# Kernel optimization log

Measured on AMD Instinct MI355X. Metric: run time of the kernel, lower is better.

## Reference

```python
import jax, jax.numpy as jnp
import numpy as np

DEPTH, HEADS, DIM_HEAD, DIM, MLP, PATCH_DIM, NP_, NC = 8, 8, 64, 512, 2048, 512, 1024, 2
INNER = HEADS * DIM_HEAD
SCALE = DIM_HEAD ** -0.5
EPS = 1e-5

def layernorm(x, s, b):
    m = x.mean(-1, keepdims=True)
    v = ((x - m) ** 2).mean(-1, keepdims=True)
    return (x - m) * jax.lax.rsqrt(v + EPS) * s + b

def setup_inputs() -> dict:
    key = jax.random.key(0)
    ks = jax.random.split(key, 24)
    g = lambda k, sh, sc=0.02: jax.random.normal(k, sh, dtype=jnp.float32) * sc
    return {
        "img": jax.random.normal(ks[0], (4, NP_, PATCH_DIM), dtype=jnp.float32),
        "embed_w": g(ks[1], (PATCH_DIM, DIM)), "embed_b": jnp.zeros((DIM,), jnp.float32),
        "pos_emb": g(ks[2], (1, NP_ + 1, DIM), 1.0), "cls_token": g(ks[3], (1, 1, DIM), 1.0),
        "ln1_s": jnp.ones((DEPTH, DIM), jnp.float32), "ln1_b": jnp.zeros((DEPTH, DIM), jnp.float32),
        "qkv_w": g(ks[4], (DEPTH, DIM, 3 * INNER)),
        "out_w": g(ks[5], (DEPTH, INNER, DIM)), "out_b": jnp.zeros((DEPTH, DIM), jnp.float32),
        "ln2_s": jnp.ones((DEPTH, DIM), jnp.float32), "ln2_b": jnp.zeros((DEPTH, DIM), jnp.float32),
        "ff_w1": g(ks[6], (DEPTH, DIM, MLP)), "ff_b1": jnp.zeros((DEPTH, MLP), jnp.float32),
        "ff_w2": g(ks[7], (DEPTH, MLP, DIM)), "ff_b2": jnp.zeros((DEPTH, DIM), jnp.float32),
        "head_ln_s": jnp.ones((DIM,), jnp.float32), "head_ln_b": jnp.zeros((DIM,), jnp.float32),
        "head_w": g(ks[8], (DIM, NC)), "head_b": jnp.zeros((NC,), jnp.float32),
    }

def reference(img, embed_w, embed_b, pos_emb, cls_token, ln1_s, ln1_b, qkv_w, out_w, out_b,
              ln2_s, ln2_b, ff_w1, ff_b1, ff_w2, ff_b2, head_ln_s, head_ln_b, head_w, head_b):
    B, N, _ = img.shape
    x = img @ embed_w + embed_b                       # [B, N, DIM]
    cls = jnp.broadcast_to(cls_token, (B, 1, DIM))
    x = jnp.concatenate([cls, x], axis=1) + pos_emb[:, :N + 1]
    for l in range(DEPTH):
        h = layernorm(x, ln1_s[l], ln1_b[l])
        qkv = h @ qkv_w[l]                            # [B, N+1, 3*INNER]
        q, k, v = jnp.split(qkv, 3, axis=-1)
        rh = lambda t: t.reshape(B, N + 1, HEADS, DIM_HEAD).transpose(0, 2, 1, 3)
        q, k, v = rh(q), rh(k), rh(v)                 # [B, H, N+1, Dh]
        dots = jnp.einsum('bhnd,bhmd->bhnm', q, k) * SCALE
        attn = jax.nn.softmax(dots, axis=-1)
        o = jnp.einsum('bhnm,bhmd->bhnd', attn, v)
        o = o.transpose(0, 2, 1, 3).reshape(B, N + 1, INNER)
        x = o @ out_w[l] + out_b[l] + x
        h = layernorm(x, ln2_s[l], ln2_b[l])
        h = jax.nn.gelu(h @ ff_w1[l] + ff_b1[l], approximate=False)
        x = h @ ff_w2[l] + ff_b2[l] + x
    x = x[:, 0]                                       # cls pooling
    x = layernorm(x, head_ln_s, head_ln_b)
    return (jax.nn.sigmoid(x @ head_w + head_b),)
```

## Files before the change

### kernel.cpp

```cpp
#include <hip/hip_runtime.h>
#include <math.h>
#include <stdint.h>

#define NHEADS   8
#define DHEAD    64
#define DIMM     512
#define MLPD     2048
#define NPATCH   1024
#define NTOK     1025
#define BATCH    4
#define ROWS     (BATCH*NTOK)
#define TOKPAD   1088
#define NCHUNK   17
#define CSPLIT   9
#define QSC      0.180336881f
#define LN_EPS   1e-5f

typedef __attribute__((ext_vector_type(8))) short short8;
typedef __attribute__((ext_vector_type(4))) float f32x4;

__device__ __forceinline__ unsigned short f2bf(float f) {
  union { float f; unsigned u; } c; c.f = f;
  unsigned u = c.u;
  return (unsigned short)((u + 0x7fffu + ((u >> 16) & 1u)) >> 16);
}
__device__ __forceinline__ unsigned short f2bf_fast(float f) {
  union { float f; unsigned u; } c; c.f = f;
  return (unsigned short)((c.u + 0x8000u) >> 16);
}
__device__ __forceinline__ float bf2f(unsigned short b) {
  union { unsigned u; float f; } c; c.u = (unsigned)b << 16;
  return c.f;
}

__device__ __forceinline__ float wsum(float v) {
#pragma unroll
  for (int o = 32; o > 0; o >>= 1) v += __shfl_xor(v, o, 64);
  return v;
}

__device__ __forceinline__ void gl_lds16(const void* g, const void* l) {
  __builtin_amdgcn_global_load_lds(
      (const __attribute__((address_space(1))) unsigned int*)(uintptr_t)g,
      (__attribute__((address_space(3))) unsigned int*)(unsigned int)(uintptr_t)l,
      16, 0, 0);
}

template <int TM, int TN, int WR, int WC>
__global__ __launch_bounds__(256) void mgemm_k(
    const unsigned short* __restrict__ A, const unsigned short* __restrict__ Bt,
    const float* __restrict__ bias, const float* __restrict__ res,
    void* __restrict__ Cout, int M, int N, int K, int flags,
    unsigned short* __restrict__ vTout)
{
  constexpr int AF = TM / WR / 16;
  constexpr int BF = TN / WC / 16;
  constexpr int AG = TM / 32;
  constexpr int BG = TN / 32;
  __shared__ unsigned short sA[2][TM * 64];
  __shared__ unsigned short sB[2][TN * 64];
  const int tid = threadIdx.x;
  const int w = tid >> 6, lane = tid & 63;
  const int quad = lane >> 4, l15 = lane & 15;
  const int m0 = blockIdx.y * TM, n0 = blockIdx.x * TN;
  const int wrow = (w / WC) * (TM / WR);
  const int wcol = (w % WC) * (TN / WC);
  const int lrow = lane >> 3;
  const int lkg = (lane & 7) ^ lrow;

  size_t abase[AG], bbase[BG];
#pragma unroll
  for (int g = 0; g < AG; g++) {
    int grp = w * AG + g;
    int ar = m0 + grp * 8 + lrow; ar = ar < M ? ar : M - 1;
    abase[g] = (size_t)ar * K + lkg * 8;
  }
#pragma unroll
  for (int g = 0; g < BG; g++) {
    int grp = w * BG + g;
    int br = n0 + grp * 8 + lrow;
    bbase[g] = (size_t)br * K + lkg * 8;
  }

  auto stage = [&](int k0, int buf) {
#pragma unroll
    for (int g = 0; g < AG; g++)
      gl_lds16(A + abase[g] + k0, &sA[buf][(w * AG + g) * 512]);
#pragma unroll
    for (int g = 0; g < BG; g++)
      gl_lds16(Bt + bbase[g] + k0, &sB[buf][(w * BG + g) * 512]);
  };

  f32x4 acc[AF][BF];
#pragma unroll
  for (int i = 0; i < AF; i++)
#pragma unroll
    for (int j = 0; j < BF; j++) { f32x4 z = {0.f, 0.f, 0.f, 0.f}; acc[i][j] = z; }

  stage(0, 0);
  const int nsteps = K >> 6;
  for (int step = 0; step < nsteps; step++) {
    const int buf = step & 1;
    __syncthreads();
    if (step + 1 < nsteps) stage((step + 1) << 6, buf ^ 1);
#pragma unroll
    for (int kk = 0; kk < 2; kk++) {
      short8 af[AF], bfr[BF];
#pragma unroll
      for (int i = 0; i < AF; i++) {
        int r = wrow + i * 16 + l15;
        af[i] = *(const short8*)&sA[buf][r * 64 + (((kk * 4 + quad) ^ (lane & 7)) << 3)];
      }
#pragma unroll
      for (int j = 0; j < BF; j++) {
        int r = wcol + j * 16 + l15;
        bfr[j] = *(const short8*)&sB[buf][r * 64 + (((kk * 4 + quad) ^ (lane & 7)) << 3)];
      }
#pragma unroll
      for (int i = 0; i < AF; i++)
#pragma unroll
        for (int j = 0; j < BF; j++)
          acc[i][j] = __builtin_amdgcn_mfma_f32_16x16x32_bf16(af[i], bfr[j], acc[i][j], 0, 0, 0);
    }
  }

  const bool do_gelu = flags & 1;
  const bool out_bf  = flags & 2;
#pragma unroll
  for (int i = 0; i < AF; i++) {
#pragma unroll
    for (int j = 0; j < BF; j++) {
      const int col = n0 + wcol + j * 16 + l15;
      const bool vcol = (vTout != nullptr) && (col >= 1024);
      alignas(8) unsigned short vb[4];
#pragma unroll
      for (int rg = 0; rg < 4; rg++) {
        int row = m0 + wrow + i * 16 + quad * 4 + rg;
        if (row >= M) continue;
        float v = acc[i][j][rg];
        if (bias) v += bias[col];
        if (do_gelu) v = 0.5f * v * (1.0f + erff(v * 0.70710678118654752f));
        if (res) v += res[(size_t)row * N + col];
        if (out_bf) {
          unsigned short bv = f2bf(v);
          vb[rg] = bv;
          if (!vcol) ((unsigned short*)Cout)[(size_t)row * N + col] = bv;
        } else {
          ((float*)Cout)[(size_t)row * N + col] = v;
        }
      }
      if (vcol) {
        const int hcol = col - 1024, h = hcol >> 6, d = hcol & 63;
#pragma unroll
        for (int rg = 0; rg < 4; rg++) {
          int row = m0 + wrow + i * 16 + quad * 4 + rg;
          if (row >= M) continue;
          int bb = row / NTOK, tok = row - bb * NTOK;
          vTout[((size_t)(bb * 8 + h) * 64 + d) * TOKPAD + tok] = vb[rg];
        }
      }
    }
  }
}

__global__ __launch_bounds__(256) void attn_k(
    const unsigned short* __restrict__ qkv, const unsigned short* __restrict__ vT,
    unsigned short* __restrict__ po, float* __restrict__ ml)
{
  __shared__ unsigned short ps[64 * 64];
  __shared__ unsigned short ks[2][64 * 64];
  __shared__ unsigned short vs[2][64 * 64];
  const int bh = blockIdx.x, b = bh >> 3, h = bh & 7;
  const int q0 = blockIdx.y * 64;
  const int split = blockIdx.z;
  const int tid = threadIdx.x, w = tid >> 6, lane = tid & 63;
  const int quad = lane >> 4, l15 = lane & 15;
  const int lrow = lane >> 3, lkg = (lane & 7) ^ lrow;
  const unsigned short* qbase = qkv + (size_t)(b * NTOK) * 1536 + h * 64;
  const unsigned short* kbase = qbase + 512;
  const unsigned short* vtb   = vT + (size_t)bh * 64 * TOKPAD;

  auto stage_kv = [&](int c0, int buf) {
#pragma unroll
    for (int g = 0; g < 2; g++) {
      int grp = w * 2 + g;
      int tok = c0 + grp * 8 + lrow; tok = tok < NTOK ? tok : NTOK - 1;
      gl_lds16(kbase + (size_t)tok * 1536 + lkg * 8, &ks[buf][grp * 512]);
      int d = grp * 8 + lrow;
      gl_lds16(vtb + (size_t)d * TOKPAD + c0 + lkg * 8, &vs[buf][grp * 512]);
    }
  };

  const int cbeg = split ? CSPLIT : 0;
  const int cend = split ? NCHUNK : CSPLIT;
  stage_kv(cbeg * 64, 0);

  int qr = q0 + w * 16 + l15; qr = qr < NTOK ? qr : NTOK - 1;
  const unsigned short* qrow = qbase + (size_t)qr * 1536;
  short8 aq[2];
  aq[0] = *(const short8*)(qrow + quad * 8);
  aq[1] = *(const short8*)(qrow + 32 + quad * 8);
#pragma unroll
  for (int k = 0; k < 2; k++)
#pragma unroll
    for (int i = 0; i < 8; i++)
      aq[k][i] = (short)f2bf(bf2f((unsigned short)aq[k][i]) * QSC);

  short8 ones;
#pragma unroll
  for (int i = 0; i < 8; i++) ones[i] = (short)0x3F80;

  f32x4 Oa[4];
#pragma unroll
  for (int n = 0; n < 4; n++) { f32x4 z = {0.f, 0.f, 0.f, 0.f}; Oa[n] = z; }
  float lst[4] = {0.f, 0.f, 0.f, 0.f};

  for (int c = cbeg; c < cend; c++) {
    const int c0 = c * 64;
    const int buf = (c - cbeg) & 1;
    __syncthreads();
    if (c + 1 < cend) stage_kv(c0 + 64, buf ^ 1);

    f32x4 sa[4];
#pragma unroll
    for (int n = 0; n < 4; n++) {
      f32x4 s = {0.f, 0.f, 0.f, 0.f};
#pragma unroll
      for (int kk = 0; kk < 2; kk++) {
        short8 bk = *(const short8*)&ks[buf][(n * 16 + l15) * 64 + (((kk * 4 + quad) ^ (lane & 7)) << 3)];
        s = __builtin_amdgcn_mfma_f32_16x16x32_bf16(aq[kk], bk, s, 0, 0, 0);
      }
      sa[n] = s;
    }

    if (c0 + 64 > NTOK) {
#pragma unroll
      for (int n = 0; n < 4; n++) {
        bool oob = (c0 + n * 16 + l15) >= NTOK;
#pragma unroll
        for (int rg = 0; rg < 4; rg++)
          if (oob) sa[n][rg] = -1e30f;
      }
    }

#pragma unroll
    for (int n = 0; n < 4; n++)
#pragma unroll
      for (int rg = 0; rg < 4; rg++) {
        int row = w * 16 + quad * 4 + rg;
        int key = n * 16 + l15;
        ps[row * 64 + ((((key >> 3) ^ (row & 7)) & 7) << 3) + (key & 7)] =
            f2bf_fast(exp2f(sa[n][rg]));
      }

    short8 ap[2];
#pragma unroll
    for (int kk = 0; kk < 2; kk++)
      ap[kk] = *(const short8*)&ps[(w * 16 + l15) * 64 + (((kk * 4 + quad) ^ (lane & 7)) << 3)];

    f32x4 lsum = {0.f, 0.f, 0.f, 0.f};
#pragma unroll
    for (int kk = 0; kk < 2; kk++)
      lsum = __builtin_amdgcn_mfma_f32_16x16x32_bf16(ap[kk], ones, lsum, 0, 0, 0);
#pragma unroll
    for (int rg = 0; rg < 4; rg++) lst[rg] += lsum[rg];

#pragma unroll
    for (int n = 0; n < 4; n++) {
      f32x4 o = Oa[n];
#pragma unroll
      for (int kk = 0; kk < 2; kk++) {
        short8 bv = *(const short8*)&vs[buf][(n * 16 + l15) * 64 + (((kk * 4 + quad) ^ (lane & 7)) << 3)];
        o = __builtin_amdgcn_mfma_f32_16x16x32_bf16(ap[kk], bv, o, 0, 0, 0);
      }
      Oa[n] = o;
    }
  }

  unsigned short* pob = po + (size_t)split * ROWS * DIMM;
#pragma unroll
  for (int n = 0; n < 4; n++)
#pragma unroll
    for (int rg = 0; rg < 4; rg++) {
      int tok = q0 + w * 16 + quad * 4 + rg;
      if (tok < NTOK)
        pob[(size_t)(b * NTOK + tok) * DIMM + h * 64 + n * 16 + l15] = f2bf(Oa[n][rg]);
    }
  if (l15 == 0) {
#pragma unroll
    for (int rg = 0; rg < 4; rg++) {
      int tok = q0 + w * 16 + quad * 4 + rg;
      if (tok < NTOK)
        ml[(size_t)(split * 32 + bh) * NTOK + tok] = lst[rg];
    }
  }
}

__global__ __launch_bounds__(256) void acomb_k(
    const unsigned short* __restrict__ po, const float* __restrict__ ml,
    unsigned short* __restrict__ out)
{
  int idx = blockIdx.x * 256 + threadIdx.x;
  if (idx >= ROWS * 64) return;
  int row = idx >> 6, g = idx & 63;
  int h = g >> 3;
  int b = row / NTOK, tok = row - b * NTOK;
  int bh = b * 8 + h;
  float l0 = ml[(size_t)bh * NTOK + tok];
  float l1 = ml[(size_t)(32 + bh) * NTOK + tok];
  float inv = 1.0f / (l0 + l1);
  size_t off = (size_t)row * DIMM + g * 8;
  alignas(16) unsigned short a0[8], a1[8], o[8];
  *(uint4*)a0 = *(const uint4*)(po + off);
  *(uint4*)a1 = *(const uint4*)(po + (size_t)ROWS * DIMM + off);
#pragma unroll
  for (int i = 0; i < 8; i++)
    o[i] = f2bf((bf2f(a0[i]) + bf2f(a1[i])) * inv);
  *(uint4*)(out + off) = *(const uint4*)o;
}

__global__ __launch_bounds__(256) void ln_k(
    const float* __restrict__ X, const float* __restrict__ s,
    const float* __restrict__ b, unsigned short* __restrict__ Y, int nrows)
{
  const int w = threadIdx.x >> 6, lane = threadIdx.x & 63;
  const int row = blockIdx.x * 4 + w;
  if (row >= nrows) return;
  const float* x = X + (size_t)row * DIMM;
  float4 v0 = *(const float4*)(x + lane * 8);
  float4 v1 = *(const float4*)(x + lane * 8 + 4);
  float xv[8] = {v0.x, v0.y, v0.z, v0.w, v1.x, v1.y, v1.z, v1.w};
  float sum = 0.f, sq = 0.f;
#pragma unroll
  for (int i = 0; i < 8; i++) { sum += xv[i]; sq += xv[i] * xv[i]; }
  sum = wsum(sum); sq = wsum(sq);
  const float mean = sum * (1.0f / DIMM);
  const float var  = sq * (1.0f / DIMM) - mean * mean;
  const float r    = rsqrtf(var + LN_EPS);
  alignas(16) unsigned short tmp[8];
#pragma unroll
  for (int i = 0; i < 8; i++) {
    int d = lane * 8 + i;
    tmp[i] = f2bf((xv[i] - mean) * r * s[d] + b[d]);
  }
  *(uint4*)&Y[(size_t)row * DIMM + lane * 8] = *(const uint4*)tmp;
}

__global__ __launch_bounds__(256) void assemble_k(
    const float* __restrict__ emb, const float* __restrict__ cls,
    const float* __restrict__ pos, float* __restrict__ X)
{
  int idx = blockIdx.x * 256 + threadIdx.x;
  if (idx >= BATCH * NTOK * DIMM) return;
  int d = idx & (DIMM - 1);
  int t = (idx >> 9) % NTOK;
  int b = idx / (NTOK * DIMM);
  float v = (t == 0) ? cls[d] : emb[((size_t)b * NPATCH + (t - 1)) * DIMM + d];
  X[idx] = v + pos[(size_t)t * DIMM + d];
}

__global__ __launch_bounds__(256) void cast_k(
    const float* __restrict__ X, unsigned short* __restrict__ Y, int n4)
{
  int i = blockIdx.x * 256 + threadIdx.x;
  if (i >= n4) return;
  float4 v = ((const float4*)X)[i];
  alignas(8) unsigned short o[4] = {f2bf(v.x), f2bf(v.y), f2bf(v.z), f2bf(v.w)};
  ((uint2*)Y)[i] = *(const uint2*)o;
}

__global__ __launch_bounds__(256) void tcast_k(
    const float* __restrict__ W, unsigned short* __restrict__ Wt, int K, int N)
{
  __shared__ float t[32][33];
  const size_t off = (size_t)blockIdx.z * K * N;
  W += off; Wt += off;
  int n0 = blockIdx.x * 32, k0 = blockIdx.y * 32;
  int tx = threadIdx.x & 31, ty = threadIdx.x >> 5;
#pragma unroll
  for (int i = 0; i < 4; i++)
    t[ty + 8 * i][tx] = W[(size_t)(k0 + ty + 8 * i) * N + n0 + tx];
  __syncthreads();
#pragma unroll
  for (int i = 0; i < 4; i++) {
    int n = ty + 8 * i;
    Wt[(size_t)(n0 + n) * K + k0 + tx] = f2bf(t[tx][n]);
  }
}

__global__ __launch_bounds__(256) void head_k(
    const float* __restrict__ X, const float* __restrict__ s,
    const float* __restrict__ bln, const float* __restrict__ W,
    const float* __restrict__ bh, float* __restrict__ out)
{
  const int w = threadIdx.x >> 6, lane = threadIdx.x & 63;
  if (w >= BATCH) return;
  const float* x = X + (size_t)w * NTOK * DIMM;
  float4 v0 = *(const float4*)(x + lane * 8);
  float4 v1 = *(const float4*)(x + lane * 8 + 4);
  float xv[8] = {v0.x, v0.y, v0.z, v0.w, v1.x, v1.y, v1.z, v1.w};
  float sum = 0.f, sq = 0.f;
#pragma unroll
  for (int i = 0; i < 8; i++) { sum += xv[i]; sq += xv[i] * xv[i]; }
  sum = wsum(sum); sq = wsum(sq);
  const float mean = sum * (1.0f / DIMM);
  const float var  = sq * (1.0f / DIMM) - mean * mean;
  const float r    = rsqrtf(var + LN_EPS);
  float l0 = 0.f, l1 = 0.f;
#pragma unroll
  for (int i = 0; i < 8; i++) {
    int d = lane * 8 + i;
    float xn = (xv[i] - mean) * r * s[d] + bln[d];
    l0 = fmaf(xn, W[d * 2 + 0], l0);
    l1 = fmaf(xn, W[d * 2 + 1], l1);
  }
  l0 = wsum(l0); l1 = wsum(l1);
  if (lane == 0) {
    out[w * 2 + 0] = 1.0f / (1.0f + expf(-(l0 + bh[0])));
    out[w * 2 + 1] = 1.0f / (1.0f + expf(-(l1 + bh[1])));
  }
}

extern "C" void kernel_launch(void* const* d_in, const int* in_sizes, int n_in,
                              void* d_out, int out_size, void* d_ws, size_t ws_size,
                              hipStream_t stream)
{
  const float* img       = (const float*)d_in[0];
  const float* embed_w   = (const float*)d_in[1];
  const float* embed_b   = (const float*)d_in[2];
  const float* pos_emb   = (const float*)d_in[3];
  const float* cls_token = (const float*)d_in[4];
  const float* ln1_s     = (const float*)d_in[5];
  const float* ln1_b     = (const float*)d_in[6];
  const float* qkv_w     = (const float*)d_in[7];
  const float* out_w     = (const float*)d_in[8];
  const float* out_b     = (const float*)d_in[9];
  const float* ln2_s     = (const float*)d_in[10];
  const float* ln2_b     = (const float*)d_in[11];
  const float* ff_w1     = (const float*)d_in[12];
  const float* ff_b1     = (const float*)d_in[13];
  const float* ff_w2     = (const float*)d_in[14];
  const float* ff_b2     = (const float*)d_in[15];
  const float* head_ln_s = (const float*)d_in[16];
  const float* head_ln_b = (const float*)d_in[17];
  const float* head_w    = (const float*)d_in[18];
  const float* head_b    = (const float*)d_in[19];
  float* out = (float*)d_out;

  char* p = (char*)d_ws;
  auto alloc = [&](size_t bytes) { char* r = p; p += (bytes + 255) & ~(size_t)255; return r; };

  unsigned short* wt_embed = (unsigned short*)alloc((size_t)512 * 512 * 2);
  unsigned short* wt_qkv   = (unsigned short*)alloc((size_t)8 * 1536 * 512 * 2);
  unsigned short* wt_out   = (unsigned short*)alloc((size_t)8 * 512 * 512 * 2);
  unsigned short* wt_ff1   = (unsigned short*)alloc((size_t)8 * 2048 * 512 * 2);
  unsigned short* wt_ff2   = (unsigned short*)alloc((size_t)8 * 512 * 2048 * 2);
  unsigned short* img_bf   = (unsigned short*)alloc((size_t)4096 * 512 * 2);
  float*          x        = (float*)alloc((size_t)ROWS * DIMM * 4);
  unsigned short* h        = (unsigned short*)alloc((size_t)ROWS * DIMM * 2);
  unsigned short* vTb      = (unsigned short*)alloc((size_t)32 * 64 * TOKPAD * 2);
  unsigned short* po       = (unsigned short*)alloc((size_t)2 * ROWS * DIMM * 2);
  float*          mlb      = (float*)alloc((size_t)2 * 32 * NTOK * 4);
  char*           big      = alloc((size_t)ROWS * MLPD * 2);
  unsigned short* qkvb     = (unsigned short*)big;
  unsigned short* attn_out = (unsigned short*)(big + (size_t)ROWS * 1536 * 2);
  unsigned short* ffh      = (unsigned short*)big;
  float*          embuf    = (float*)big;

  dim3 blk(256);

  cast_k<<<(4096 * 512 / 4 + 255) / 256, blk, 0, stream>>>(img, img_bf, 4096 * 512 / 4);
  tcast_k<<<dim3(16, 16, 1), blk, 0, stream>>>(embed_w, wt_embed, 512, 512);
  tcast_k<<<dim3(48, 16, 8), blk, 0, stream>>>(qkv_w, wt_qkv, 512, 1536);
  tcast_k<<<dim3(16, 16, 8), blk, 0, stream>>>(out_w, wt_out, 512, 512);
  tcast_k<<<dim3(64, 16, 8), blk, 0, stream>>>(ff_w1, wt_ff1, 512, 2048);
  tcast_k<<<dim3(16, 64, 8), blk, 0, stream>>>(ff_w2, wt_ff2, 2048, 512);

  mgemm_k<64, 64, 2, 2><<<dim3(8, 64), blk, 0, stream>>>(
      img_bf, wt_embed, embed_b, nullptr, embuf, 4096, 512, 512, 0, nullptr);
  assemble_k<<<(BATCH * NTOK * DIMM + 255) / 256, blk, 0, stream>>>(
      embuf, cls_token, pos_emb, x);

  const int mt64 = (ROWS + 63) / 64;
  for (int l = 0; l < 8; l++) {
    ln_k<<<(ROWS + 3) / 4, blk, 0, stream>>>(
        x, ln1_s + l * DIMM, ln1_b + l * DIMM, h, ROWS);
    mgemm_k<64, 128, 1, 4><<<dim3(12, mt64), blk, 0, stream>>>(
        h, wt_qkv + (size_t)l * 1536 * 512, nullptr, nullptr,
        qkvb, ROWS, 1536, 512, 2, vTb);
    attn_k<<<dim3(32, 17, 2), blk, 0, stream>>>(qkvb, vTb, po, mlb);
    acomb_k<<<(ROWS * 64 + 255) / 256, blk, 0, stream>>>(po, mlb, attn_out);
    mgemm_k<64, 64, 2, 2><<<dim3(8, mt64), blk, 0, stream>>>(
        attn_out, wt_out + (size_t)l * 512 * 512, out_b + l * DIMM, x,
        x, ROWS, 512, 512, 0, nullptr);
    ln_k<<<(ROWS + 3) / 4, blk, 0, stream>>>(
        x, ln2_s + l * DIMM, ln2_b + l * DIMM, h, ROWS);
    mgemm_k<64, 128, 1, 4><<<dim3(16, mt64), blk, 0, stream>>>(
        h, wt_ff1 + (size_t)l * 2048 * 512, ff_b1 + l * MLPD, nullptr,
        ffh, ROWS, 2048, 512, 1 | 2, nullptr);
    mgemm_k<64, 64, 2, 2><<<dim3(8, mt64), blk, 0, stream>>>(
        ffh, wt_ff2 + (size_t)l * 512 * 2048, ff_b2 + l * DIMM, x,
        x, ROWS, 512, 2048, 0, nullptr);
  }

  head_k<<<1, blk, 0, stream>>>(x, head_ln_s, head_ln_b, head_w, head_b, out);
}
```

Baseline: 1.303 ms.

## Fuse attention split-combine into out-projection GEMM A-tile loading

Drops the separate acomb_k kernel, which merged the two attention split partials and normalised them by the summed row sums. The out-projection GEMM now loads both partial outputs and their normaliser values into registers, combines them, and writes the result into LDS itself, with the loads software-pipelined across the MFMA loop. This saves one kernel launch and one write-then-read of the combined activation buffer per layer. In exchange the A operand goes through registers instead of direct global-to-LDS DMA, each block fetches twice the A bytes plus scattered normaliser loads and does divides, and register pressure rises.

```diff
diff --git a/kernel.cpp b/kernel.cpp
--- a/kernel.cpp
+++ b/kernel.cpp
@@ -46,12 +46,12 @@
       16, 0, 0);
 }
 
-template <int TM, int TN, int WR, int WC>
+template <int TM, int TN, int WR, int WC, bool ACOMB>
 __global__ __launch_bounds__(256) void mgemm_k(
     const unsigned short* __restrict__ A, const unsigned short* __restrict__ Bt,
     const float* __restrict__ bias, const float* __restrict__ res,
     void* __restrict__ Cout, int M, int N, int K, int flags,
-    unsigned short* __restrict__ vTout)
+    unsigned short* __restrict__ vTout, const float* __restrict__ mlc)
 {
   constexpr int AF = TM / WR / 16;
   constexpr int BF = TN / WC / 16;
@@ -69,10 +69,12 @@
   const int lkg = (lane & 7) ^ lrow;
 
   size_t abase[AG], bbase[BG];
+  int arow[AG];
 #pragma unroll
   for (int g = 0; g < AG; g++) {
     int grp = w * AG + g;
     int ar = m0 + grp * 8 + lrow; ar = ar < M ? ar : M - 1;
+    arow[g] = ar;
     abase[g] = (size_t)ar * K + lkg * 8;
   }
 #pragma unroll
@@ -82,14 +84,45 @@
     bbase[g] = (size_t)br * K + lkg * 8;
   }
 
-  auto stage = [&](int k0, int buf) {
-#pragma unroll
-    for (int g = 0; g < AG; g++)
-      gl_lds16(A + abase[g] + k0, &sA[buf][(w * AG + g) * 512]);
+  auto stageB = [&](int k0, int buf) {
 #pragma unroll
     for (int g = 0; g < BG; g++)
       gl_lds16(Bt + bbase[g] + k0, &sB[buf][(w * BG + g) * 512]);
   };
+  auto stageA_dma = [&](int k0, int buf) {
+#pragma unroll
+    for (int g = 0; g < AG; g++)
+      gl_lds16(A + abase[g] + k0, &sA[buf][(w * AG + g) * 512]);
+  };
+
+  uint4 ra0[AG], ra1[AG];
+  float rl0[AG], rl1[AG];
+  auto loadA = [&](int k0) {
+    const int h = k0 >> 6;
+#pragma unroll
+    for (int g = 0; g < AG; g++) {
+      size_t off = abase[g] + k0;
+      ra0[g] = *(const uint4*)(A + off);
+      ra1[g] = *(const uint4*)(A + (size_t)ROWS * DIMM + off);
+      int b = arow[g] / NTOK, tok = arow[g] - b * NTOK;
+      int bh = b * 8 + h;
+      rl0[g] = mlc[(size_t)bh * NTOK + tok];
+      rl1[g] = mlc[(size_t)(32 + bh) * NTOK + tok];
+    }
+  };
+  auto writeA = [&](int buf) {
+#pragma unroll
+    for (int g = 0; g < AG; g++) {
+      float inv = 1.0f / (rl0[g] + rl1[g]);
+      const unsigned short* p0 = (const unsigned short*)&ra0[g];
+      const unsigned short* p1 = (const unsigned short*)&ra1[g];
+      alignas(16) unsigned short o[8];
+#pragma unroll
+      for (int i = 0; i < 8; i++)
+        o[i] = f2bf((bf2f(p0[i]) + bf2f(p1[i])) * inv);
+      *(uint4*)&sA[buf][(w * AG + g) * 512 + lane * 8] = *(const uint4*)o;
+    }
+  };
 
   f32x4 acc[AF][BF];
 #pragma unroll
@@ -97,12 +130,18 @@
 #pragma unroll
     for (int j = 0; j < BF; j++) { f32x4 z = {0.f, 0.f, 0.f, 0.f}; acc[i][j] = z; }
 
-  stage(0, 0);
+  if (ACOMB) { stageB(0, 0); loadA(0); writeA(0); }
+  else       { stageA_dma(0, 0); stageB(0, 0); }
+
   const int nsteps = K >> 6;
   for (int step = 0; step < nsteps; step++) {
     const int buf = step & 1;
     __syncthreads();
-    if (step + 1 < nsteps) stage((step + 1) << 6, buf ^ 1);
+    if (step + 1 < nsteps) {
+      stageB((step + 1) << 6, buf ^ 1);
+      if (ACOMB) loadA((step + 1) << 6);
+      else       stageA_dma((step + 1) << 6, buf ^ 1);
+    }
 #pragma unroll
     for (int kk = 0; kk < 2; kk++) {
       short8 af[AF], bfr[BF];
@@ -122,6 +161,7 @@
         for (int j = 0; j < BF; j++)
           acc[i][j] = __builtin_amdgcn_mfma_f32_16x16x32_bf16(af[i], bfr[j], acc[i][j], 0, 0, 0);
     }
+    if (ACOMB && step + 1 < nsteps) writeA(buf ^ 1);
   }
 
   const bool do_gelu = flags & 1;
@@ -294,29 +334,6 @@
         ml[(size_t)(split * 32 + bh) * NTOK + tok] = lst[rg];
     }
   }
-}
-
-__global__ __launch_bounds__(256) void acomb_k(
-    const unsigned short* __restrict__ po, const float* __restrict__ ml,
-    unsigned short* __restrict__ out)
-{
-  int idx = blockIdx.x * 256 + threadIdx.x;
-  if (idx >= ROWS * 64) return;
-  int row = idx >> 6, g = idx & 63;
-  int h = g >> 3;
-  int b = row / NTOK, tok = row - b * NTOK;
-  int bh = b * 8 + h;
-  float l0 = ml[(size_t)bh * NTOK + tok];
-  float l1 = ml[(size_t)(32 + bh) * NTOK + tok];
-  float inv = 1.0f / (l0 + l1);
-  size_t off = (size_t)row * DIMM + g * 8;
-  alignas(16) unsigned short a0[8], a1[8], o[8];
-  *(uint4*)a0 = *(const uint4*)(po + off);
-  *(uint4*)a1 = *(const uint4*)(po + (size_t)ROWS * DIMM + off);
-#pragma unroll
-  for (int i = 0; i < 8; i++)
-    o[i] = f2bf((bf2f(a0[i]) + bf2f(a1[i])) * inv);
-  *(uint4*)(out + off) = *(const uint4*)o;
 }
 
 __global__ __launch_bounds__(256) void ln_k(
@@ -463,7 +480,6 @@
   float*          mlb      = (float*)alloc((size_t)2 * 32 * NTOK * 4);
   char*           big      = alloc((size_t)ROWS * MLPD * 2);
   unsigned short* qkvb     = (unsigned short*)big;
-  unsigned short* attn_out = (unsigned short*)(big + (size_t)ROWS * 1536 * 2);
   unsigned short* ffh      = (unsigned short*)big;
   float*          embuf    = (float*)big;
 
@@ -476,8 +492,8 @@
   tcast_k<<<dim3(64, 16, 8), blk, 0, stream>>>(ff_w1, wt_ff1, 512, 2048);
   tcast_k<<<dim3(16, 64, 8), blk, 0, stream>>>(ff_w2, wt_ff2, 2048, 512);
 
-  mgemm_k<64, 64, 2, 2><<<dim3(8, 64), blk, 0, stream>>>(
-      img_bf, wt_embed, embed_b, nullptr, embuf, 4096, 512, 512, 0, nullptr);
+  mgemm_k<64, 64, 2, 2, false><<<dim3(8, 64), blk, 0, stream>>>(
+      img_bf, wt_embed, embed_b, nullptr, embuf, 4096, 512, 512, 0, nullptr, nullptr);
   assemble_k<<<(BATCH * NTOK * DIMM + 255) / 256, blk, 0, stream>>>(
       embuf, cls_token, pos_emb, x);
 
@@ -485,22 +501,21 @@
   for (int l = 0; l < 8; l++) {
     ln_k<<<(ROWS + 3) / 4, blk, 0, stream>>>(
         x, ln1_s + l * DIMM, ln1_b + l * DIMM, h, ROWS);
-    mgemm_k<64, 128, 1, 4><<<dim3(12, mt64), blk, 0, stream>>>(
+    mgemm_k<64, 128, 1, 4, false><<<dim3(12, mt64), blk, 0, stream>>>(
         h, wt_qkv + (size_t)l * 1536 * 512, nullptr, nullptr,
-        qkvb, ROWS, 1536, 512, 2, vTb);
+        qkvb, ROWS, 1536, 512, 2, vTb, nullptr);
     attn_k<<<dim3(32, 17, 2), blk, 0, stream>>>(qkvb, vTb, po, mlb);
-    acomb_k<<<(ROWS * 64 + 255) / 256, blk, 0, stream>>>(po, mlb, attn_out);
-    mgemm_k<64, 64, 2, 2><<<dim3(8, mt64), blk, 0, stream>>>(
-        attn_out, wt_out + (size_t)l * 512 * 512, out_b + l * DIMM, x,
-        x, ROWS, 512, 512, 0, nullptr);
+    mgemm_k<64, 64, 2, 2, true><<<dim3(8, mt64), blk, 0, stream>>>(
+        po, wt_out + (size_t)l * 512 * 512, out_b + l * DIMM, x,
+        x, ROWS, 512, 512, 0, nullptr, mlb);
     ln_k<<<(ROWS + 3) / 4, blk, 0, stream>>>(
         x, ln2_s + l * DIMM, ln2_b + l * DIMM, h, ROWS);
-    mgemm_k<64, 128, 1, 4><<<dim3(16, mt64), blk, 0, stream>>>(
+    mgemm_k<64, 128, 1, 4, false><<<dim3(16, mt64), blk, 0, stream>>>(
         h, wt_ff1 + (size_t)l * 2048 * 512, ff_b1 + l * MLPD, nullptr,
-        ffh, ROWS, 2048, 512, 1 | 2, nullptr);
-    mgemm_k<64, 64, 2, 2><<<dim3(8, mt64), blk, 0, stream>>>(
+        ffh, ROWS, 2048, 512, 1 | 2, nullptr, nullptr);
+    mgemm_k<64, 64, 2, 2, false><<<dim3(8, mt64), blk, 0, stream>>>(
         ffh, wt_ff2 + (size_t)l * 512 * 2048, ff_b2 + l * DIMM, x,
-        x, ROWS, 512, 2048, 0, nullptr);
+        x, ROWS, 512, 2048, 0, nullptr, nullptr);
   }
 
   head_k<<<1, blk, 0, stream>>>(x, head_ln_s, head_ln_b, head_w, head_b, out);
```

Result: no change. 1.304 ms (+0.1%).
